# Performance work log

Measured on AMD Instinct MI355X. Metric: run time of the kernel, lower is better.

## Reference

```python
import jax, jax.numpy as jnp
import numpy as np

NUM_CLUSTERS = 64  # real clusters (ghost clusters excluded from residuals)
EPS = 1e-12        # F.normalize eps


def setup_inputs() -> dict:
    key = jax.random.key(0)
    k1, k2, k3 = jax.random.split(key, 3)
    x = jax.random.normal(k1, (8, 128, 32, 32), dtype=jnp.float32)
    # 1x1 conv weight [K+G, C] (kernel spatial dims squeezed), no bias (vladv2=False)
    conv_w = jax.random.normal(k2, (68, 128), dtype=jnp.float32) * 0.05
    centroids = jax.random.uniform(k3, (68, 128), dtype=jnp.float32)
    return {"x": x, "conv_w": conv_w, "centroids": centroids}


def reference(x, conv_w, centroids):
    # x: [N,C,H,W]; conv_w: [K+G,C]; centroids: [K+G,C]
    # descriptor-wise L2 normalization over channel dim (normalize_input=True)
    nrm = jnp.sqrt(jnp.sum(x * x, axis=1, keepdims=True))
    xn = x / jnp.maximum(nrm, EPS)
    # 1x1 conv -> soft assignment logits over K+G clusters, softmax over cluster dim
    logits = jnp.einsum('nchw,kc->nkhw', xn, conv_w)
    soft_assign = jax.nn.softmax(logits, axis=1)            # [N,K+G,H,W]
    # fused per-cluster residual: (x - c_k) * a_k, only real clusters
    resid = (xn[:, None, :, :, :] -
             centroids[:NUM_CLUSTERS][None, :, :, None, None])  # [N,K,C,H,W]
    store_residual = resid * soft_assign[:, :NUM_CLUSTERS, None, :, :]
    return store_residual, soft_assign
```

## Files before the change

kernel.cpp:

```cpp
#include <hip/hip_runtime.h>

#define PIMG 1024
#define CCH  128
#define KG   68
#define KR   64
#define T1   32
#define XP   36
#define WP   132
#define LP   36

typedef float f4v __attribute__((ext_vector_type(4)));

__global__ __launch_bounds__(512) void nv_fused_kernel(
    const float* __restrict__ x,
    const float* __restrict__ conv_w,
    const float* __restrict__ centroids,
    float* __restrict__ out,
    float* __restrict__ sa_out)
{
    __shared__ float xs[CCH * XP];
    __shared__ float wl[KG * WP];
    __shared__ float lg[KG * LP];
    __shared__ float red[16 * T1];
    __shared__ float rn_l[T1];
    __shared__ float mx_l[T1];
    __shared__ float is_l[T1];

    const int t   = threadIdx.x;
    const int gp0 = blockIdx.x * T1;
    const int n   = gp0 >> 10;
    const int p0  = gp0 & 1023;

    for (int i = t; i < KG * (CCH / 4); i += 512) {
        int k = i >> 5, c4 = i & 31;
        *(f4v*)(wl + k * WP + c4 * 4) = ((const f4v*)(conv_w + k * CCH))[c4];
    }
    const float* xb = x + (size_t)n * (CCH * PIMG) + p0;
    for (int i = t; i < CCH * T1; i += 512) {
        int c = i >> 5, pix = i & 31;
        xs[c * XP + pix] = xb[c * PIMG + pix];
    }
    __syncthreads();

    {
        int pix = t & 31, q = t >> 5;
        float s = 0.f;
        #pragma unroll
        for (int c = q * 8; c < q * 8 + 8; ++c) {
            float v = xs[c * XP + pix];
            s += v * v;
        }
        red[q * T1 + pix] = s;
    }
    __syncthreads();
    if (t < T1) {
        float s = 0.f;
        #pragma unroll
        for (int q = 0; q < 16; ++q) s += red[q * T1 + t];
        rn_l[t] = 1.0f / fmaxf(sqrtf(s), 1e-12f);
    }
    __syncthreads();
    for (int i = t; i < CCH * T1; i += 512) {
        int pix = i & 31;
        xs[(i >> 5) * XP + pix] *= rn_l[pix];
    }
    __syncthreads();

    if (t < 136) {
        const int g = t & 7, q = t >> 3;
        const float* xr = xs + g * 4;
        const float* w0 = wl + q * WP;
        const float* w1 = wl + (q + 17) * WP;
        const float* w2 = wl + (q + 34) * WP;
        const float* w3 = wl + (q + 51) * WP;
        f4v a0 = {0,0,0,0}, a1 = {0,0,0,0}, a2 = {0,0,0,0}, a3 = {0,0,0,0};
        #pragma unroll 8
        for (int c0 = 0; c0 < CCH; c0 += 4) {
            f4v x0 = *(const f4v*)(xr + (c0 + 0) * XP);
            f4v x1 = *(const f4v*)(xr + (c0 + 1) * XP);
            f4v x2 = *(const f4v*)(xr + (c0 + 2) * XP);
            f4v x3 = *(const f4v*)(xr + (c0 + 3) * XP);
            f4v v0 = *(const f4v*)(w0 + c0);
            f4v v1 = *(const f4v*)(w1 + c0);
            f4v v2 = *(const f4v*)(w2 + c0);
            f4v v3 = *(const f4v*)(w3 + c0);
            a0 += x0 * v0.x; a0 += x1 * v0.y; a0 += x2 * v0.z; a0 += x3 * v0.w;
            a1 += x0 * v1.x; a1 += x1 * v1.y; a1 += x2 * v1.z; a1 += x3 * v1.w;
            a2 += x0 * v2.x; a2 += x1 * v2.y; a2 += x2 * v2.z; a2 += x3 * v2.w;
            a3 += x0 * v3.x; a3 += x1 * v3.y; a3 += x2 * v3.z; a3 += x3 * v3.w;
        }
        *(f4v*)(lg + q * LP + g * 4)        = a0;
        *(f4v*)(lg + (q + 17) * LP + g * 4) = a1;
        *(f4v*)(lg + (q + 34) * LP + g * 4) = a2;
        *(f4v*)(lg + (q + 51) * LP + g * 4) = a3;
    }
    __syncthreads();

    {
        int pix = t & 31, q = t >> 5;
        float m = -1e30f;
        for (int k = q; k < KG; k += 16) m = fmaxf(m, lg[k * LP + pix]);
        red[q * T1 + pix] = m;
    }
    __syncthreads();
    if (t < T1) {
        float m = red[t];
        #pragma unroll
        for (int q = 1; q < 16; ++q) m = fmaxf(m, red[q * T1 + t]);
        mx_l[t] = m;
    }
    __syncthreads();
    {
        int pix = t & 31, q = t >> 5;
        float m = mx_l[pix], s = 0.f;
        for (int k = q; k < KG; k += 16) {
            float e = expf(lg[k * LP + pix] - m);
            lg[k * LP + pix] = e;
            s += e;
        }
        red[q * T1 + pix] = s;
    }
    __syncthreads();
    if (t < T1) {
        float s = 0.f;
        #pragma unroll
        for (int q = 0; q < 16; ++q) s += red[q * T1 + t];
        is_l[t] = 1.0f / s;
    }
    __syncthreads();

    for (int i = t; i < KG * T1; i += 512) {
        int k = i >> 5, pix = i & 31;
        float v = lg[k * LP + pix] * is_l[pix];
        lg[k * LP + pix] = v;
        sa_out[((size_t)n * KG + k) * PIMG + p0 + pix] = v;
    }
    __syncthreads();

    {
        const int g  = t & 7;
        const int cp = t >> 3;
        const int c0 = 2 * cp, c1 = 2 * cp + 1;
        const f4v xn0 = *(const f4v*)(xs + c0 * XP + g * 4);
        const f4v xn1 = *(const f4v*)(xs + c1 * XP + g * 4);
        const float* cb = centroids;
        float* ob = out + (size_t)n * (KR * CCH * PIMG) + p0 + g * 4;

        #pragma unroll 4
        for (int k = 0; k < KR; ++k) {
            f4v a4 = *(const f4v*)(lg + k * LP + g * 4);
            float ce0 = cb[k * CCH + c0];
            float ce1 = cb[k * CCH + c1];
            *(f4v*)(ob + ((size_t)k * CCH + c0) * PIMG) = (xn0 - ce0) * a4;
            *(f4v*)(ob + ((size_t)k * CCH + c1) * PIMG) = (xn1 - ce1) * a4;
        }
    }
}

extern "C" void kernel_launch(void* const* d_in, const int* in_sizes, int n_in,
                              void* d_out, int out_size, void* d_ws, size_t ws_size,
                              hipStream_t stream) {
    const float* x         = (const float*)d_in[0];
    const float* conv_w    = (const float*)d_in[1];
    const float* centroids = (const float*)d_in[2];

    const int N = in_sizes[0] / (CCH * PIMG);

    float* out    = (float*)d_out;
    float* sa_out = out + (size_t)N * KR * CCH * PIMG;

    nv_fused_kernel<<<N * (PIMG / T1), 512, 0, stream>>>(
        x, conv_w, centroids, out, sa_out);
}
```

Baseline: 54.11 us.

## Widen pixel tile to 64 and split residual clusters across two blocks

Each block now handles 64 pixels and half of the 64 real clusters, so the grid stays at 256 blocks while every block writes 256-byte contiguous output rows. The conv-weight shared-memory staging is removed and weights are read straight from global/L1. The norm pass is fused with the x load. Each pixel tile's normalization and logits are now computed twice (once per cluster half), with only one half writing soft_assign. That redundant compute and the uncached weight reads are the price.

```diff
diff --git a/kernel.cpp b/kernel.cpp
--- a/kernel.cpp
+++ b/kernel.cpp
@@ -4,10 +4,9 @@
 #define CCH  128
 #define KG   68
 #define KR   64
-#define T1   32
-#define XP   36
-#define WP   132
-#define LP   36
+#define T1   64
+#define XP   68
+#define LP   68
 
 typedef float f4v __attribute__((ext_vector_type(4)));
 
@@ -19,60 +18,57 @@
     float* __restrict__ sa_out)
 {
     __shared__ float xs[CCH * XP];
-    __shared__ float wl[KG * WP];
     __shared__ float lg[KG * LP];
-    __shared__ float red[16 * T1];
+    __shared__ float red[8 * T1];
     __shared__ float rn_l[T1];
     __shared__ float mx_l[T1];
     __shared__ float is_l[T1];
 
-    const int t   = threadIdx.x;
-    const int gp0 = blockIdx.x * T1;
-    const int n   = gp0 >> 10;
-    const int p0  = gp0 & 1023;
-
-    for (int i = t; i < KG * (CCH / 4); i += 512) {
-        int k = i >> 5, c4 = i & 31;
-        *(f4v*)(wl + k * WP + c4 * 4) = ((const f4v*)(conv_w + k * CCH))[c4];
-    }
-    const float* xb = x + (size_t)n * (CCH * PIMG) + p0;
-    for (int i = t; i < CCH * T1; i += 512) {
-        int c = i >> 5, pix = i & 31;
-        xs[c * XP + pix] = xb[c * PIMG + pix];
-    }
-    __syncthreads();
+    const int t    = threadIdx.x;
+    const int b    = blockIdx.x;
+    const int kh   = b & 1;
+    const int tile = (b >> 1) & 15;
+    const int n    = b >> 5;
+    const int p0   = tile * T1;
+    const int k0   = kh * 32;
 
     {
-        int pix = t & 31, q = t >> 5;
-        float s = 0.f;
+        const int pix = t & 63, cg = t >> 6;
+        const float* xb = x + (size_t)n * (CCH * PIMG) + p0 + pix;
+        float ss = 0.f;
         #pragma unroll
-        for (int c = q * 8; c < q * 8 + 8; ++c) {
-            float v = xs[c * XP + pix];
-            s += v * v;
+        for (int j = 0; j < 16; ++j) {
+            int c = cg + 8 * j;
+            float v = xb[(size_t)c * PIMG];
+            xs[c * XP + pix] = v;
+            ss += v * v;
         }
-        red[q * T1 + pix] = s;
+        red[cg * T1 + pix] = ss;
     }
     __syncthreads();
     if (t < T1) {
         float s = 0.f;
         #pragma unroll
-        for (int q = 0; q < 16; ++q) s += red[q * T1 + t];
+        for (int q = 0; q < 8; ++q) s += red[q * T1 + t];
         rn_l[t] = 1.0f / fmaxf(sqrtf(s), 1e-12f);
     }
     __syncthreads();
-    for (int i = t; i < CCH * T1; i += 512) {
-        int pix = i & 31;
-        xs[(i >> 5) * XP + pix] *= rn_l[pix];
+    {
+        const int pix = t & 63, cg = t >> 6;
+        const float r = rn_l[pix];
+        #pragma unroll
+        for (int j = 0; j < 16; ++j)
+            xs[(cg + 8 * j) * XP + pix] *= r;
     }
     __syncthreads();
 
-    if (t < 136) {
-        const int g = t & 7, q = t >> 3;
+    if (t < 272) {
+        const int g = t & 15, q = t >> 4;
         const float* xr = xs + g * 4;
-        const float* w0 = wl + q * WP;
-        const float* w1 = wl + (q + 17) * WP;
-        const float* w2 = wl + (q + 34) * WP;
-        const float* w3 = wl + (q + 51) * WP;
+        const float* w0 = conv_w + q * CCH;
+        const float* w1 = conv_w + (q + 17) * CCH;
+        const float* w2 = conv_w + (q + 34) * CCH;
+        const float* w3 = conv_w + (q + 51) * CCH;
         f4v a0 = {0,0,0,0}, a1 = {0,0,0,0}, a2 = {0,0,0,0}, a3 = {0,0,0,0};
         #pragma unroll 8
         for (int c0 = 0; c0 < CCH; c0 += 4) {
@@ -97,23 +93,24 @@
     __syncthreads();
 
     {
-        int pix = t & 31, q = t >> 5;
+        const int pix = t & 63, q = t >> 6;
         float m = -1e30f;
-        for (int k = q; k < KG; k += 16) m = fmaxf(m, lg[k * LP + pix]);
+        for (int k = q; k < KG; k += 8) m = fmaxf(m, lg[k * LP + pix]);
         red[q * T1 + pix] = m;
     }
     __syncthreads();
     if (t < T1) {
         float m = red[t];
         #pragma unroll
-        for (int q = 1; q < 16; ++q) m = fmaxf(m, red[q * T1 + t]);
+        for (int q = 1; q < 8; ++q) m = fmaxf(m, red[q * T1 + t]);
         mx_l[t] = m;
     }
     __syncthreads();
     {
-        int pix = t & 31, q = t >> 5;
-        float m = mx_l[pix], s = 0.f;
-        for (int k = q; k < KG; k += 16) {
+        const int pix = t & 63, q = t >> 6;
+        const float m = mx_l[pix];
+        float s = 0.f;
+        for (int k = q; k < KG; k += 8) {
             float e = expf(lg[k * LP + pix] - m);
             lg[k * LP + pix] = e;
             s += e;
@@ -124,35 +121,40 @@
     if (t < T1) {
         float s = 0.f;
         #pragma unroll
-        for (int q = 0; q < 16; ++q) s += red[q * T1 + t];
+        for (int q = 0; q < 8; ++q) s += red[q * T1 + t];
         is_l[t] = 1.0f / s;
     }
     __syncthreads();
 
     for (int i = t; i < KG * T1; i += 512) {
-        int k = i >> 5, pix = i & 31;
+        int k = i >> 6, pix = i & 63;
         float v = lg[k * LP + pix] * is_l[pix];
         lg[k * LP + pix] = v;
-        sa_out[((size_t)n * KG + k) * PIMG + p0 + pix] = v;
+        if (kh == 0)
+            sa_out[((size_t)n * KG + k) * PIMG + p0 + pix] = v;
     }
     __syncthreads();
 
     {
-        const int g  = t & 7;
-        const int cp = t >> 3;
-        const int c0 = 2 * cp, c1 = 2 * cp + 1;
-        const f4v xn0 = *(const f4v*)(xs + c0 * XP + g * 4);
-        const f4v xn1 = *(const f4v*)(xs + c1 * XP + g * 4);
-        const float* cb = centroids;
-        float* ob = out + (size_t)n * (KR * CCH * PIMG) + p0 + g * 4;
+        const int g  = t & 15;
+        const int cq = t >> 4;
+        f4v xn[4];
+        #pragma unroll
+        for (int j = 0; j < 4; ++j)
+            xn[j] = *(const f4v*)(xs + (4 * cq + j) * XP + g * 4);
+
+        const float* cb = centroids + (size_t)k0 * CCH + 4 * cq;
+        float* ob = out + (((size_t)n * KR + k0) * CCH) * PIMG + p0 + g * 4;
 
         #pragma unroll 4
-        for (int k = 0; k < KR; ++k) {
-            f4v a4 = *(const f4v*)(lg + k * LP + g * 4);
-            float ce0 = cb[k * CCH + c0];
-            float ce1 = cb[k * CCH + c1];
-            *(f4v*)(ob + ((size_t)k * CCH + c0) * PIMG) = (xn0 - ce0) * a4;
-            *(f4v*)(ob + ((size_t)k * CCH + c1) * PIMG) = (xn1 - ce1) * a4;
+        for (int k = 0; k < 32; ++k) {
+            f4v a4 = *(const f4v*)(lg + (k0 + k) * LP + g * 4);
+            #pragma unroll
+            for (int j = 0; j < 4; ++j) {
+                float ce = cb[k * CCH + j];
+                *(f4v*)(ob + ((size_t)k * CCH + 4 * cq + j) * PIMG) =
+                    (xn[j] - ce) * a4;
+            }
         }
     }
 }
@@ -169,6 +171,6 @@
     float* out    = (float*)d_out;
     float* sa_out = out + (size_t)N * KR * CCH * PIMG;
 
-    nv_fused_kernel<<<N * (PIMG / T1), 512, 0, stream>>>(
+    nv_fused_kernel<<<N * 16 * 2, 512, 0, stream>>>(
         x, conv_w, centroids, out, sa_out);
 }
```

Result: slower. 56.48 us (+4.4%).
